# Kernel optimization log

Hardware: AMD Instinct MI355X
Metric: run time of the kernel (lower is better)

## Reference

```python
import jax, jax.numpy as jnp
import numpy as np

EPS = 1e-5


def setup_inputs() -> dict:
    key = jax.random.key(0)
    ks = jax.random.split(key, 8)
    B, C, D, H, O, E = 256, 64, 256, 4096, 256, 4
    x = jax.random.normal(ks[0], (B, C, D), dtype=jnp.float32)
    mask_ids = jax.random.randint(ks[1], (B, C), 0, 16)
    projection_idx = jax.random.randint(ks[2], (C,), 0, E)
    W1 = jax.random.normal(ks[3], (E, D, H), dtype=jnp.float32) * 0.02
    b1 = jnp.zeros((E, H), dtype=jnp.float32)
    gamma = jnp.ones((E, H), dtype=jnp.float32)
    beta = jnp.zeros((E, H), dtype=jnp.float32)
    W2 = jax.random.normal(ks[4], (E, H, O), dtype=jnp.float32) * 0.02
    b2 = jnp.zeros((E, O), dtype=jnp.float32)
    return {"x": x, "mask_ids": mask_ids, "projection_idx": projection_idx,
            "W1": W1, "b1": b1, "gamma": gamma, "beta": beta, "W2": W2, "b2": b2}


def reference(x, mask_ids, projection_idx, W1, b1, gamma, beta, W2, b2):
    # x: [B, C, D]; projection_idx: [C] routes each channel to one of E experts.
    # Disjoint masks => the original zeros + masked '+=' is a partition-assign.
    B, C, D = x.shape
    E, _, H = W1.shape
    # Per-channel expert params (gather once, shared over batch).
    h = jnp.einsum('bcd,cdh->bch', x, W1[projection_idx]) + b1[projection_idx]
    # BatchNorm1d in training mode: batch stats over the tokens of each expert
    # (the original flattens the selected [B, |mask|] tokens for BN).
    seg = jnp.broadcast_to(projection_idx[None, :], (B, C)).reshape(-1)  # [B*C]
    hf = h.reshape(B * C, H)
    cnt = jax.ops.segment_sum(jnp.ones((B * C,), h.dtype), seg, num_segments=E)
    cnt = jnp.maximum(cnt, 1.0)
    s1 = jax.ops.segment_sum(hf, seg, num_segments=E)            # [E, H]
    s2 = jax.ops.segment_sum(hf * hf, seg, num_segments=E)       # [E, H]
    mean = s1 / cnt[:, None]
    var = s2 / cnt[:, None] - mean * mean                        # biased var (train-mode BN)
    inv = jax.lax.rsqrt(var + EPS)
    hn = (h - mean[projection_idx]) * (inv[projection_idx] * gamma[projection_idx]) + beta[projection_idx]
    a = jax.nn.relu(hn)
    out = jnp.einsum('bch,cho->bco', a, W2[projection_idx]) + b2[projection_idx]
    return out, mask_ids
```

## Files before the change

### kernel.cpp

```cpp
#include <hip/hip_runtime.h>

typedef unsigned short u16;
typedef unsigned int   u32;
typedef __attribute__((ext_vector_type(8))) short s16x8;
typedef __attribute__((ext_vector_type(4))) float f32x4;
typedef __attribute__((ext_vector_type(4))) u32   u32x4;

#define DEV static __device__ __forceinline__

static constexpr int B_ = 256, C_ = 64, D_ = 256, H_ = 4096, O_ = 256, E_ = 4;

DEV u16 f2bf(float f) {
  u32 u = __builtin_bit_cast(u32, f);
  u += 0x7fffu + ((u >> 16) & 1u);
  return (u16)(u >> 16);
}
DEV float bf2f(u16 u) { return __builtin_bit_cast(float, (u32)u << 16); }

DEV void async16(const u16* g, u16* l) {
  __builtin_amdgcn_global_load_lds(
      (const __attribute__((address_space(1))) void*)g,
      (__attribute__((address_space(3))) void*)l, 16, 0, 0);
}

DEV int xcd_swz(int bid, int nwg) { return (bid & 7) * (nwg >> 3) + (bid >> 3); }

__global__ void k_prep(const float* __restrict__ x, u16* __restrict__ xb,
                       const float* __restrict__ W1, u16* __restrict__ w1t,
                       const float* __restrict__ W2, u16* __restrict__ w2t,
                       const int* __restrict__ proj, int* __restrict__ perm) {
  __shared__ float tile[64][65];
  const int bx = blockIdx.x, tid = threadIdx.x;
  if (bx < 2048) {
    const int i = bx * 256 + tid;
    const f32x4 a = ((const f32x4*)x)[2 * i];
    const f32x4 b = ((const f32x4*)x)[2 * i + 1];
    u32x4 o;
    o[0] = (u32)f2bf(a[0]) | ((u32)f2bf(a[1]) << 16);
    o[1] = (u32)f2bf(a[2]) | ((u32)f2bf(a[3]) << 16);
    o[2] = (u32)f2bf(b[0]) | ((u32)f2bf(b[1]) << 16);
    o[3] = (u32)f2bf(b[2]) | ((u32)f2bf(b[3]) << 16);
    ((u32x4*)xb)[i] = o;
    return;
  }
  if (bx < 4096) {
    const bool w1 = bx < 3072;
    const int R  = w1 ? D_ : H_;
    const int Cc = w1 ? H_ : O_;
    const float* s0 = w1 ? W1 : W2;
    u16* d0 = w1 ? w1t : w2t;
    int b = bx - (w1 ? 2048 : 3072);
    const int nct = Cc >> 6, nrt = R >> 6;
    const int ct = b % nct; b /= nct;
    const int rt = b % nrt; const int e = b / nrt;
    const float* s = s0 + (size_t)e * R * Cc;
    u16* d = d0 + (size_t)e * R * Cc;
    const int tx = tid & 63, ty = tid >> 6;
    #pragma unroll
    for (int i = 0; i < 64; i += 4)
      tile[i + ty][tx] = s[(size_t)(rt * 64 + i + ty) * Cc + ct * 64 + tx];
    __syncthreads();
    #pragma unroll
    for (int i = 0; i < 64; i += 4) {
      const int cc = i + ty;
      d[(size_t)(ct * 64 + cc) * R + rt * 64 + tx] = f2bf(tile[tx][cc]);
    }
    return;
  }
  if (tid < C_) {
    const int e = proj[tid];
    int rank = 0;
    for (int c2 = 0; c2 < C_; ++c2) {
      const int e2 = proj[c2];
      rank += (e2 < e) || (e2 == e && c2 < tid);
    }
    perm[rank] = tid;
  }
}

__global__ __launch_bounds__(256, 4)
void k_gemm1(const u16* __restrict__ A, const u16* __restrict__ Bw,
             const int* __restrict__ proj, const int* __restrict__ perm,
             const float* __restrict__ bias,
             u16* __restrict__ outH, float* __restrict__ s1g, float* __restrict__ s2g) {
  constexpr int BM = 128, BN = 128, BK = 32, KT = D_ / BK;
  constexpr int SA = BM * BK / 8, SB = BN * BK / 8;
  constexpr int BUF = (SA + SB) * 8;
  __shared__ __align__(16) u16 lds[2 * BUF];
  const int tid = threadIdx.x, l = tid & 63, w = tid >> 6, wm = w >> 1, wn = w & 1;

  int bid = xcd_swz(blockIdx.x, gridDim.x);
  constexpr int NT = H_ / BN, BT = B_ / BM;
  const int nt = bid % NT; bid /= NT;
  const int bt = bid % BT; const int ci = bid / BT;
  const int c = perm[ci];
  const int e = proj[c];

  const size_t rsA = (size_t)C_ * D_;
  const u16* Ab = A + (size_t)c * D_ + (size_t)bt * BM * rsA;
  const u16* Bb = Bw + ((size_t)e * H_ + (size_t)nt * BN) * D_;

  f32x4 acc[4][4] = {};

  auto stage = [&](int kt) {
    const int k0 = kt * BK;
    u16* dst = lds + (kt & 1) * BUF;
    #pragma unroll
    for (int i = 0; i < 2; ++i) {
      const int s = i * 256 + tid, row = s >> 2, j = (s & 3) ^ ((row >> 1) & 3);
      async16(Ab + (size_t)row * rsA + k0 + j * 8, dst + s * 8);
    }
    #pragma unroll
    for (int i = 0; i < 2; ++i) {
      const int s = i * 256 + tid, col = s >> 2, j = (s & 3) ^ ((col >> 1) & 3);
      async16(Bb + (size_t)col * D_ + k0 + j * 8, dst + SA * 8 + s * 8);
    }
  };

  stage(0);
  asm volatile("s_waitcnt vmcnt(0)" ::: "memory");
  __builtin_amdgcn_s_barrier();

  #pragma unroll
  for (int kt = 0; kt < KT; ++kt) {
    if (kt + 1 < KT) stage(kt + 1);
    const u16* bufA = lds + (kt & 1) * BUF;
    const u16* bufB = bufA + SA * 8;
    s16x8 av[4], bv[4];
    #pragma unroll
    for (int m = 0; m < 4; ++m) {
      const int r = wm * 64 + m * 16 + (l & 15), p = (l >> 4) ^ ((r >> 1) & 3);
      av[m] = *(const s16x8*)(bufA + (r * 4 + p) * 8);
    }
    #pragma unroll
    for (int n = 0; n < 4; ++n) {
      const int cc = wn * 64 + n * 16 + (l & 15), p = (l >> 4) ^ ((cc >> 1) & 3);
      bv[n] = *(const s16x8*)(bufB + (cc * 4 + p) * 8);
    }
    #pragma unroll
    for (int m = 0; m < 4; ++m)
      #pragma unroll
      for (int n = 0; n < 4; ++n)
        acc[m][n] = __builtin_amdgcn_mfma_f32_16x16x32_bf16(av[m], bv[n], acc[m][n], 0, 0, 0);
    asm volatile("s_waitcnt vmcnt(0) lgkmcnt(0)" ::: "memory");
    __builtin_amdgcn_s_barrier();
  }

  u16* ldsOut = lds;
  #pragma unroll
  for (int n = 0; n < 4; ++n) {
    const int colL = wn * 64 + n * 16 + (l & 15);
    const int colg = nt * BN + colL;
    const float bval = bias[e * H_ + colg];
    float p1 = 0.f, p2 = 0.f;
    #pragma unroll
    for (int m = 0; m < 4; ++m) {
      const int rbase = wm * 64 + m * 16 + (l >> 4) * 4;
      #pragma unroll
      for (int i = 0; i < 4; ++i) {
        const float v = acc[m][n][i] + bval;
        p1 += v; p2 += v * v;
        const int row = rbase + i;
        const int phys = (colL >> 3) ^ (row & 15);
        ldsOut[row * 128 + phys * 8 + (colL & 7)] = f2bf(v);
      }
    }
    p1 += __shfl_xor(p1, 16); p1 += __shfl_xor(p1, 32);
    p2 += __shfl_xor(p2, 16); p2 += __shfl_xor(p2, 32);
    if (l < 16) {
      atomicAdd(&s1g[e * H_ + colg], p1);
      atomicAdd(&s2g[e * H_ + colg], p2);
    }
  }
  __syncthreads();
  u16* outB = outH + ((size_t)(bt * BM) * C_ + c) * H_ + nt * BN;
  #pragma unroll
  for (int pass = 0; pass < 8; ++pass) {
    const int row = pass * 16 + (tid >> 4), sl = tid & 15;
    const u32x4 v = *(const u32x4*)(ldsOut + row * 128 + ((sl ^ (row & 15)) * 8));
    *(u32x4*)(outB + (size_t)row * C_ * H_ + sl * 8) = v;
  }
}

__global__ void k_finalize(const float* __restrict__ s1, const float* __restrict__ s2,
                           const int* __restrict__ proj, const float* __restrict__ gamma,
                           const float* __restrict__ beta,
                           u16* __restrict__ sclB, u16* __restrict__ shfB) {
  const int i = blockIdx.x * 256 + threadIdx.x;
  const int e = i >> 12;
  int cn = 0;
  #pragma unroll
  for (int c = 0; c < C_; ++c) cn += (proj[c] == e) ? 1 : 0;
  const float cnt = fmaxf((float)cn * (float)B_, 1.f);
  const float mean = s1[i] / cnt;
  const float var = s2[i] / cnt - mean * mean;
  const float sc = rsqrtf(var + 1e-5f) * gamma[i];
  sclB[i] = f2bf(sc);
  shfB[i] = f2bf(beta[i] - mean * sc);
}

template<int KS>
__global__ __launch_bounds__(256, 4)
void k_gemm2(const u16* __restrict__ A, const u16* __restrict__ Bw,
             const int* __restrict__ proj, const int* __restrict__ perm,
             const float* __restrict__ b2,
             const u16* __restrict__ scB, const u16* __restrict__ shB,
             float* __restrict__ outF, float* __restrict__ partial) {
  constexpr int BM = 128, BN = 128, BK = 32, KH = H_ / KS, KT = KH / BK;
  constexpr int SA = BM * BK / 8, SB = BN * BK / 8;
  constexpr int BUF = (SA + SB) * 8;
  __shared__ __align__(16) u16 lds[2 * BUF + 2 * KH];
  u16* stS = lds + 2 * BUF;
  u16* stT = stS + KH;
  const int tid = threadIdx.x, l = tid & 63, w = tid >> 6, wm = w >> 1, wn = w & 1;

  int bid = xcd_swz(blockIdx.x, gridDim.x);
  const int ks = bid & (KS - 1); bid /= KS;
  const int nt = bid & 1; bid >>= 1;
  const int bt = bid & 1; const int ci = bid >> 1;
  const int c = perm[ci];
  const int e = proj[c];

  const size_t rsA = (size_t)C_ * H_;
  const u16* Ab = A + (size_t)c * H_ + (size_t)bt * BM * rsA + (size_t)ks * KH;
  const u16* Bb = Bw + ((size_t)e * O_ + (size_t)nt * BN) * H_ + (size_t)ks * KH;
  const u16* scE = scB + e * H_ + ks * KH;
  const u16* shE = shB + e * H_ + ks * KH;

  f32x4 acc[4][4] = {};
  s16x8 h0[2], h1[2], b0r[2], b1r[2];

  auto Aissue = [&](int kt, s16x8 (&hs)[2]) {
    const int k0 = kt * BK;
    #pragma unroll
    for (int i = 0; i < 2; ++i) {
      const int s = i * 256 + tid, row = s >> 2, j = (s & 3) ^ ((row >> 1) & 3);
      hs[i] = *(const s16x8*)(Ab + (size_t)row * rsA + k0 + j * 8);
    }
  };
  auto Bissue = [&](int kt, s16x8 (&bs)[2]) {
    const int k0 = kt * BK;
    #pragma unroll
    for (int i = 0; i < 2; ++i) {
      const int s = i * 256 + tid, col = s >> 2, j = (s & 3) ^ ((col >> 1) & 3);
      bs[i] = *(const s16x8*)(Bb + (size_t)col * H_ + k0 + j * 8);
    }
  };
  auto Awrite = [&](int kt, s16x8 (&hs)[2]) {
    u16* dst = lds + (kt & 1) * BUF;
    const int k0 = kt * BK;
    #pragma unroll
    for (int i = 0; i < 2; ++i) {
      const int s = i * 256 + tid, row = s >> 2, j = (s & 3) ^ ((row >> 1) & 3);
      const s16x8 sv = *(const s16x8*)(stS + k0 + j * 8);
      const s16x8 tv = *(const s16x8*)(stT + k0 + j * 8);
      u32x4 o;
      #pragma unroll
      for (int jj = 0; jj < 4; ++jj) {
        const float v0 = fmaxf(bf2f((u16)hs[i][2 * jj]) * bf2f((u16)sv[2 * jj]) + bf2f((u16)tv[2 * jj]), 0.f);
        const float v1 = fmaxf(bf2f((u16)hs[i][2 * jj + 1]) * bf2f((u16)sv[2 * jj + 1]) + bf2f((u16)tv[2 * jj + 1]), 0.f);
        o[jj] = (u32)f2bf(v0) | ((u32)f2bf(v1) << 16);
      }
      *(u32x4*)(dst + s * 8) = o;
    }
  };
  auto Bwrite = [&](int kt, s16x8 (&bs)[2]) {
    u16* dst = lds + (kt & 1) * BUF + SA * 8;
    #pragma unroll
    for (int i = 0; i < 2; ++i) {
      const int s = i * 256 + tid;
      *(u32x4*)(dst + s * 8) = __builtin_bit_cast(u32x4, bs[i]);
    }
  };
  auto Compute = [&](int kt) {
    const u16* bufA = lds + (kt & 1) * BUF;
    const u16* bufB = bufA + SA * 8;
    s16x8 av[4], bv[4];
    #pragma unroll
    for (int m = 0; m < 4; ++m) {
      const int r = wm * 64 + m * 16 + (l & 15), p = (l >> 4) ^ ((r >> 1) & 3);
      av[m] = *(const s16x8*)(bufA + (r * 4 + p) * 8);
    }
    #pragma unroll
    for (int n = 0; n < 4; ++n) {
      const int cc = wn * 64 + n * 16 + (l & 15), p = (l >> 4) ^ ((cc >> 1) & 3);
      bv[n] = *(const s16x8*)(bufB + (cc * 4 + p) * 8);
    }
    #pragma unroll
    for (int m = 0; m < 4; ++m)
      #pragma unroll
      for (int n = 0; n < 4; ++n)
        acc[m][n] = __builtin_amdgcn_mfma_f32_16x16x32_bf16(av[m], bv[n], acc[m][n], 0, 0, 0);
  };

  for (int q = tid; q < KH / 4; q += 256) {
    if (q < KH / 8) async16(scE + q * 8, stS + q * 8);
    else            async16(shE + (q - KH / 8) * 8, stT + (q - KH / 8) * 8);
  }
  Aissue(0, h0); Bissue(0, b0r);
  Aissue(1, h1); Bissue(1, b1r);
  asm volatile("s_waitcnt vmcnt(0)" ::: "memory");
  __builtin_amdgcn_s_barrier();
  Awrite(0, h0); Bwrite(0, b0r);
  asm volatile("s_waitcnt lgkmcnt(0)" ::: "memory");
  __builtin_amdgcn_s_barrier();

  #pragma unroll 1
  for (int kt = 0; kt + 3 < KT; kt += 2) {
    Aissue(kt + 2, h0); Bissue(kt + 2, b0r);
    Compute(kt);
    Awrite(kt + 1, h1); Bwrite(kt + 1, b1r);
    asm volatile("s_waitcnt lgkmcnt(0)" ::: "memory");
    __builtin_amdgcn_s_barrier();
    Aissue(kt + 3, h1); Bissue(kt + 3, b1r);
    Compute(kt + 1);
    Awrite(kt + 2, h0); Bwrite(kt + 2, b0r);
    asm volatile("s_waitcnt lgkmcnt(0)" ::: "memory");
    __builtin_amdgcn_s_barrier();
  }

  Compute(KT - 2);
  Awrite(KT - 1, h1); Bwrite(KT - 1, b1r);
  asm volatile("s_waitcnt lgkmcnt(0)" ::: "memory");
  __builtin_amdgcn_s_barrier();
  Compute(KT - 1);

  float* dstF = ks ? (partial + (size_t)(ks - 1) * B_ * C_ * O_) : outF;
  #pragma unroll
  for (int n = 0; n < 4; ++n) {
    const int colg = nt * BN + wn * 64 + n * 16 + (l & 15);
    const float bval = ks ? 0.f : b2[e * O_ + colg];
    #pragma unroll
    for (int m = 0; m < 4; ++m) {
      #pragma unroll
      for (int i = 0; i < 4; ++i) {
        const int rg = bt * BM + wm * 64 + m * 16 + (l >> 4) * 4 + i;
        dstF[((size_t)rg * C_ + c) * O_ + colg] = acc[m][n][i] + bval;
      }
    }
  }
}

__global__ void k_combine(float* __restrict__ out, const float* __restrict__ partial,
                          const int nparts, const int* __restrict__ mask,
                          float* __restrict__ maskOut) {
  const int gi = blockIdx.x * 256 + threadIdx.x;
  const size_t b = (size_t)gi * 2;
  constexpr size_t PARTV = (size_t)B_ * C_ * O_ / 4;
  f32x4 a0 = ((const f32x4*)out)[b], a1 = ((const f32x4*)out)[b + 1];
  for (int p = 0; p < nparts; ++p) {
    const f32x4 p0 = ((const f32x4*)partial)[p * PARTV + b];
    const f32x4 p1 = ((const f32x4*)partial)[p * PARTV + b + 1];
    #pragma unroll
    for (int j = 0; j < 4; ++j) { a0[j] += p0[j]; a1[j] += p1[j]; }
  }
  ((f32x4*)out)[b] = a0; ((f32x4*)out)[b + 1] = a1;
  if (gi < B_ * C_ / 8) {
    #pragma unroll
    for (int j = 0; j < 8; ++j) maskOut[gi * 8 + j] = (float)mask[gi * 8 + j];
  }
}

extern "C" void kernel_launch(void* const* d_in, const int* in_sizes, int n_in,
                              void* d_out, int out_size, void* d_ws, size_t ws_size,
                              hipStream_t stream) {
  const float* x     = (const float*)d_in[0];
  const int*   mask  = (const int*)d_in[1];
  const int*   proj  = (const int*)d_in[2];
  const float* W1    = (const float*)d_in[3];
  const float* b1    = (const float*)d_in[4];
  const float* gamma = (const float*)d_in[5];
  const float* beta  = (const float*)d_in[6];
  const float* W2    = (const float*)d_in[7];
  const float* b2    = (const float*)d_in[8];
  float* out = (float*)d_out;

  char* ws = (char*)d_ws;
  size_t off = 0;
  u16* hbuf = (u16*)(ws + off); off += (size_t)B_ * C_ * H_ * 2;
  u16* xb   = (u16*)(ws + off); off += (size_t)B_ * C_ * D_ * 2;
  u16* w1t  = (u16*)(ws + off); off += (size_t)E_ * D_ * H_ * 2;
  float* partial2 = (float*)xb;
  u16* w2t  = (u16*)(ws + off); off += (size_t)E_ * H_ * O_ * 2;
  float* s1 = (float*)(ws + off); off += (size_t)E_ * H_ * 4;
  float* s2 = (float*)(ws + off); off += (size_t)E_ * H_ * 4;
  u16* sclB = (u16*)(ws + off); off += (size_t)E_ * H_ * 2;
  u16* shfB = (u16*)(ws + off); off += (size_t)E_ * H_ * 2;
  int* perm = (int*)(ws + off); off += 256;
  off = (off + 255) & ~(size_t)255;
  float* partial4 = (float*)(ws + off);
  const bool ks4 = ws_size >= off + (size_t)3 * B_ * C_ * O_ * 4;

  (void)hipMemsetAsync(s1, 0, (size_t)2 * E_ * H_ * 4, stream);

  k_prep<<<4097, 256, 0, stream>>>(x, xb, W1, w1t, W2, w2t, proj, perm);

  k_gemm1<<<C_ * 2 * 32, 256, 0, stream>>>(xb, w1t, proj, perm, b1, hbuf, s1, s2);

  k_finalize<<<E_ * H_ / 256, 256, 0, stream>>>(s1, s2, proj, gamma, beta, sclB, shfB);

  if (ks4) {
    k_gemm2<4><<<1024, 256, 0, stream>>>(hbuf, w2t, proj, perm, b2, sclB, shfB, out, partial4);
    k_combine<<<B_ * C_ * O_ / 8 / 256, 256, 0, stream>>>(out, partial4, 3, mask,
                                                          out + (size_t)B_ * C_ * O_);
  } else {
    k_gemm2<2><<<512, 256, 0, stream>>>(hbuf, w2t, proj, perm, b2, sclB, shfB, out, partial2);
    k_combine<<<B_ * C_ * O_ / 8 / 256, 256, 0, stream>>>(out, partial2, 1, mask,
                                                          out + (size_t)B_ * C_ * O_);
  }
}
```

Baseline: 183.0 us.

## Replace BN stat atomics with per-tile partial sums and channel-major hidden layout

Per-column BatchNorm sums in gemm1 are no longer accumulated with global float atomics. Each tile now combines its two warp-row halves through shared memory and writes non-atomic partials indexed by (channel, batch-tile). The finalize kernel reduces those partials per expert, which removes the memset and atomic contention at the cost of more partial-sum reads there. The hidden activation buffer also switches to a channel-major [C][B][H] layout, so gemm1 output rows and gemm2 A rows are contiguous with stride H instead of C*H.

```diff
diff --git a/kernel.cpp b/kernel.cpp
--- a/kernel.cpp
+++ b/kernel.cpp
@@ -82,11 +82,12 @@
 void k_gemm1(const u16* __restrict__ A, const u16* __restrict__ Bw,
              const int* __restrict__ proj, const int* __restrict__ perm,
              const float* __restrict__ bias,
-             u16* __restrict__ outH, float* __restrict__ s1g, float* __restrict__ s2g) {
+             u16* __restrict__ outH, float* __restrict__ s1p, float* __restrict__ s2p) {
   constexpr int BM = 128, BN = 128, BK = 32, KT = D_ / BK;
   constexpr int SA = BM * BK / 8, SB = BN * BK / 8;
   constexpr int BUF = (SA + SB) * 8;
   __shared__ __align__(16) u16 lds[2 * BUF];
+  __shared__ float stash[2][4][16][2];
   const int tid = threadIdx.x, l = tid & 63, w = tid >> 6, wm = w >> 1, wn = w & 1;
 
   int bid = xcd_swz(blockIdx.x, gridDim.x);
@@ -147,6 +148,7 @@
   }
 
   u16* ldsOut = lds;
+  float p1s[4], p2s[4];
   #pragma unroll
   for (int n = 0; n < 4; ++n) {
     const int colL = wn * 64 + n * 16 + (l & 15);
@@ -167,33 +169,47 @@
     }
     p1 += __shfl_xor(p1, 16); p1 += __shfl_xor(p1, 32);
     p2 += __shfl_xor(p2, 16); p2 += __shfl_xor(p2, 32);
-    if (l < 16) {
-      atomicAdd(&s1g[e * H_ + colg], p1);
-      atomicAdd(&s2g[e * H_ + colg], p2);
-    }
+    if (wm == 1 && l < 16) { stash[wn][n][l & 15][0] = p1; stash[wn][n][l & 15][1] = p2; }
+    p1s[n] = p1; p2s[n] = p2;
   }
   __syncthreads();
-  u16* outB = outH + ((size_t)(bt * BM) * C_ + c) * H_ + nt * BN;
+  if (wm == 0 && l < 16) {
+    const int rowp = c * 2 + bt;
+    #pragma unroll
+    for (int n = 0; n < 4; ++n) {
+      const int colg = nt * BN + wn * 64 + n * 16 + (l & 15);
+      s1p[(size_t)rowp * H_ + colg] = p1s[n] + stash[wn][n][l & 15][0];
+      s2p[(size_t)rowp * H_ + colg] = p2s[n] + stash[wn][n][l & 15][1];
+    }
+  }
+  u16* outB = outH + ((size_t)c * B_ + (size_t)bt * BM) * H_ + nt * BN;
   #pragma unroll
   for (int pass = 0; pass < 8; ++pass) {
     const int row = pass * 16 + (tid >> 4), sl = tid & 15;
     const u32x4 v = *(const u32x4*)(ldsOut + row * 128 + ((sl ^ (row & 15)) * 8));
-    *(u32x4*)(outB + (size_t)row * C_ * H_ + sl * 8) = v;
-  }
-}
-
-__global__ void k_finalize(const float* __restrict__ s1, const float* __restrict__ s2,
+    *(u32x4*)(outB + (size_t)row * H_ + sl * 8) = v;
+  }
+}
+
+__global__ void k_finalize(const float* __restrict__ s1p, const float* __restrict__ s2p,
                            const int* __restrict__ proj, const float* __restrict__ gamma,
                            const float* __restrict__ beta,
                            u16* __restrict__ sclB, u16* __restrict__ shfB) {
   const int i = blockIdx.x * 256 + threadIdx.x;
   const int e = i >> 12;
+  const int hcol = i & 4095;
   int cn = 0;
-  #pragma unroll
-  for (int c = 0; c < C_; ++c) cn += (proj[c] == e) ? 1 : 0;
+  float q1 = 0.f, q2 = 0.f;
+  for (int c = 0; c < C_; ++c) {
+    if (proj[c] == e) {
+      ++cn;
+      q1 += s1p[(size_t)(c * 2) * H_ + hcol] + s1p[(size_t)(c * 2 + 1) * H_ + hcol];
+      q2 += s2p[(size_t)(c * 2) * H_ + hcol] + s2p[(size_t)(c * 2 + 1) * H_ + hcol];
+    }
+  }
   const float cnt = fmaxf((float)cn * (float)B_, 1.f);
-  const float mean = s1[i] / cnt;
-  const float var = s2[i] / cnt - mean * mean;
+  const float mean = q1 / cnt;
+  const float var = q2 / cnt - mean * mean;
   const float sc = rsqrtf(var + 1e-5f) * gamma[i];
   sclB[i] = f2bf(sc);
   shfB[i] = f2bf(beta[i] - mean * sc);
@@ -221,8 +237,8 @@
   const int c = perm[ci];
   const int e = proj[c];
 
-  const size_t rsA = (size_t)C_ * H_;
-  const u16* Ab = A + (size_t)c * H_ + (size_t)bt * BM * rsA + (size_t)ks * KH;
+  const size_t rsA = (size_t)H_;
+  const u16* Ab = A + ((size_t)c * B_ + (size_t)bt * BM) * H_ + (size_t)ks * KH;
   const u16* Bb = Bw + ((size_t)e * O_ + (size_t)nt * BN) * H_ + (size_t)ks * KH;
   const u16* scE = scB + e * H_ + ks * KH;
   const u16* shE = shB + e * H_ + ks * KH;
@@ -382,8 +398,8 @@
   u16* w1t  = (u16*)(ws + off); off += (size_t)E_ * D_ * H_ * 2;
   float* partial2 = (float*)xb;
   u16* w2t  = (u16*)(ws + off); off += (size_t)E_ * H_ * O_ * 2;
-  float* s1 = (float*)(ws + off); off += (size_t)E_ * H_ * 4;
-  float* s2 = (float*)(ws + off); off += (size_t)E_ * H_ * 4;
+  float* s1p = (float*)(ws + off); off += (size_t)2 * C_ * H_ * 4;
+  float* s2p = (float*)(ws + off); off += (size_t)2 * C_ * H_ * 4;
   u16* sclB = (u16*)(ws + off); off += (size_t)E_ * H_ * 2;
   u16* shfB = (u16*)(ws + off); off += (size_t)E_ * H_ * 2;
   int* perm = (int*)(ws + off); off += 256;
@@ -391,13 +407,12 @@
   float* partial4 = (float*)(ws + off);
   const bool ks4 = ws_size >= off + (size_t)3 * B_ * C_ * O_ * 4;
 
-  (void)hipMemsetAsync(s1, 0, (size_t)2 * E_ * H_ * 4, stream);
 
   k_prep<<<4097, 256, 0, stream>>>(x, xb, W1, w1t, W2, w2t, proj, perm);
 
-  k_gemm1<<<C_ * 2 * 32, 256, 0, stream>>>(xb, w1t, proj, perm, b1, hbuf, s1, s2);
-
-  k_finalize<<<E_ * H_ / 256, 256, 0, stream>>>(s1, s2, proj, gamma, beta, sclB, shfB);
+  k_gemm1<<<C_ * 2 * 32, 256, 0, stream>>>(xb, w1t, proj, perm, b1, hbuf, s1p, s2p);
+
+  k_finalize<<<E_ * H_ / 256, 256, 0, stream>>>(s1p, s2p, proj, gamma, beta, sclB, shfB);
 
   if (ks4) {
     k_gemm2<4><<<1024, 256, 0, stream>>>(hbuf, w2t, proj, perm, b2, sclB, shfB, out, partial4);
```

New measurement: 177.8 us. 1.03x faster.
